# Optimization experiments

Hardware: AMD Instinct MI355X
Metric: run time of the kernel (lower is better)

The kernel has to match this reference:

```python
import jax, jax.numpy as jnp
import numpy as np

# Config (matches init_kwargs)
D_MODEL = 1024
D_MLP = 4096
N_EXPERTS = 8
TOP_K = 2  # experts_per_token
BATCH = 1
POS = 2048


def setup_inputs() -> dict:
    key = jax.random.key(0)
    k0, k1, k2, k3, k4 = jax.random.split(key, 5)
    s = 0.02  # typical init scale
    x = jax.random.normal(k0, (BATCH, POS, D_MODEL), jnp.float32)
    W_gate = jax.random.normal(k1, (D_MODEL, N_EXPERTS), jnp.float32) * s  # router
    We_gate = jax.random.normal(k2, (N_EXPERTS, D_MODEL, D_MLP), jnp.float32) * s
    We_in = jax.random.normal(k3, (N_EXPERTS, D_MODEL, D_MLP), jnp.float32) * s
    We_out = jax.random.normal(k4, (N_EXPERTS, D_MLP, D_MODEL), jnp.float32) * s
    return {"x": x, "W_gate": W_gate, "We_gate": We_gate, "We_in": We_in, "We_out": We_out}


def reference(x, W_gate, We_gate, We_in, We_out):
    B, P, D = x.shape
    T = B * P
    E = W_gate.shape[1]
    h = x.reshape(T, D)  # [T, D]

    # Router: logits -> fp32 softmax -> top-k -> renormalize (as in torch code)
    logits = h @ W_gate  # [T, E]
    probs = jax.nn.softmax(logits.astype(jnp.float32), axis=-1)
    topw, topi = jax.lax.top_k(probs, TOP_K)  # [T, K]
    topw = topw / jnp.sum(topw, axis=-1, keepdims=True)
    topw = topw.astype(x.dtype)

    # Per-token combine weight for each expert (0 if not routed). [T, E]
    w_full = jnp.zeros((T, E), x.dtype).at[jnp.arange(T)[:, None], topi].add(topw)

    # Gated-MLP per expert; scan over the small fixed expert axis to avoid
    # materializing [E, T, D_MLP] hidden states at once.
    def per_expert(acc, params):
        Wg, Wi, Wo, we = params  # Wg/Wi: [D, D_MLP], Wo: [D_MLP, D], we: [T]
        hid = jax.nn.silu(h @ Wg) * (h @ Wi)  # [T, D_MLP]
        return acc + (hid @ Wo) * we[:, None], None

    res, _ = jax.lax.scan(
        per_expert,
        jnp.zeros((T, D), x.dtype),
        (We_gate, We_in, We_out, w_full.T),
    )
    return res.reshape(B, P, D)
```

## Files before the change

kernel.cpp:

```cpp
#include <hip/hip_runtime.h>
#include <hip/hip_bf16.h>

#define T_TOK 2048
#define DMODEL 1024
#define DMLP 4096
#define NEXP 8
#define YB 4

typedef __bf16 bf16x8 __attribute__((ext_vector_type(8)));
typedef float f32x4 __attribute__((ext_vector_type(4)));
typedef unsigned short u16x8 __attribute__((ext_vector_type(8)));

__device__ __forceinline__ unsigned short f2bf(float f) {
  return __builtin_bit_cast(unsigned short, (__bf16)f);
}

__global__ __launch_bounds__(64) void router_k(
    const float* __restrict__ x, const float* __restrict__ wg,
    int* __restrict__ topi, float* __restrict__ topw) {
  int t = blockIdx.x;
  int lane = threadIdx.x;
  const float* hx = x + (size_t)t * DMODEL;
  float acc[NEXP];
#pragma unroll
  for (int e = 0; e < NEXP; ++e) acc[e] = 0.f;
  for (int i = lane; i < DMODEL; i += 64) {
    float xi = hx[i];
    const float* w = wg + (size_t)i * NEXP;
#pragma unroll
    for (int e = 0; e < NEXP; ++e) acc[e] += xi * w[e];
  }
#pragma unroll
  for (int off = 32; off > 0; off >>= 1) {
#pragma unroll
    for (int e = 0; e < NEXP; ++e) acc[e] += __shfl_down(acc[e], off);
  }
  if (lane == 0) {
    float m = acc[0];
#pragma unroll
    for (int e = 1; e < NEXP; ++e) m = fmaxf(m, acc[e]);
    float p[NEXP], s = 0.f;
#pragma unroll
    for (int e = 0; e < NEXP; ++e) { p[e] = expf(acc[e] - m); s += p[e]; }
    float inv = 1.f / s;
#pragma unroll
    for (int e = 0; e < NEXP; ++e) p[e] *= inv;
    int i1 = 0;
#pragma unroll
    for (int e = 1; e < NEXP; ++e) if (p[e] > p[i1]) i1 = e;
    int i2 = (i1 == 0) ? 1 : 0;
#pragma unroll
    for (int e = 0; e < NEXP; ++e) if (e != i1 && p[e] > p[i2]) i2 = e;
    float w1 = p[i1], w2 = p[i2];
    float rs = 1.f / (w1 + w2);
    topi[2 * t] = i1;
    topi[2 * t + 1] = i2;
    topw[2 * t] = w1 * rs;
    topw[2 * t + 1] = w2 * rs;
  }
}

__global__ __launch_bounds__(512) void compact_k(
    const int* __restrict__ topi, const float* __restrict__ topw,
    int* __restrict__ offsets, int* __restrict__ perm,
    float* __restrict__ wrow) {
  int tid = threadIdx.x;
  int w = tid >> 6, lane = tid & 63;
  __shared__ int hist[NEXP][NEXP];
  __shared__ int base_s[NEXP][NEXP];
  unsigned long long ltmask = (lane == 63) ? ~0ULL >> 1 : ((1ULL << lane) - 1ULL);

  int c[NEXP];
#pragma unroll
  for (int ex = 0; ex < NEXP; ++ex) c[ex] = 0;
  for (int it = 0; it < 8; ++it) {
    int j = w * 512 + it * 64 + lane;
    int e = topi[j];
#pragma unroll
    for (int ex = 0; ex < NEXP; ++ex) {
      unsigned long long m = __ballot(e == ex);
      c[ex] += __popcll(m);
    }
  }
  if (lane == 0) {
#pragma unroll
    for (int ex = 0; ex < NEXP; ++ex) hist[w][ex] = c[ex];
  }
  __syncthreads();
  if (tid == 0) {
    int s = 0;
    for (int ex = 0; ex < NEXP; ++ex) {
      offsets[ex] = s;
      int t = s;
      for (int w2 = 0; w2 < NEXP; ++w2) { base_s[w2][ex] = t; t += hist[w2][ex]; }
      s = t;
    }
    offsets[NEXP] = s;
  }
  __syncthreads();
  int rb[NEXP];
#pragma unroll
  for (int ex = 0; ex < NEXP; ++ex) rb[ex] = base_s[w][ex];
  for (int it = 0; it < 8; ++it) {
    int j = w * 512 + it * 64 + lane;
    int e = topi[j];
    float pw = topw[j];
#pragma unroll
    for (int ex = 0; ex < NEXP; ++ex) {
      unsigned long long m = __ballot(e == ex);
      if (e == ex) {
        int p = rb[ex] + __popcll(m & ltmask);
        perm[p] = j >> 1;
        wrow[p] = pw;
      }
      rb[ex] += __popcll(m);
    }
  }
}

#define BPITCH 40

__global__ __launch_bounds__(256) void hid_k(
    const float* __restrict__ x, const float* __restrict__ weg,
    const float* __restrict__ wei, const int* __restrict__ offsets,
    const int* __restrict__ perm, const float* __restrict__ wrow,
    unsigned short* __restrict__ hid) {
  int e = blockIdx.z;
  int off = offsets[e], cnt = offsets[e + 1] - off;
  int nb = blockIdx.x * 64;
  const float* wg = weg + (size_t)e * DMODEL * DMLP;
  const float* wi = wei + (size_t)e * DMODEL * DMLP;

  __shared__ unsigned short As[128 * BPITCH];
  __shared__ unsigned short Bg[64 * BPITCH];
  __shared__ unsigned short Bi[64 * BPITCH];

  int tid = threadIdx.x;
  int lane = tid & 63, wid = tid >> 6;
  int wm = (wid & 1) * 64, wn = (wid >> 1) * 32;
  int lr = lane & 15, q = lane >> 4;

  int bn = tid & 63, kq = tid >> 6;
  const float* gsrc = wg + (size_t)(kq * 8) * DMLP + nb + bn;
  const float* isrc = wi + (size_t)(kq * 8) * DMLP + nb + bn;
  int bdst = bn * BPITCH + kq * 8;

  for (int m0 = blockIdx.y * 128; m0 < cnt; m0 += YB * 128) {
    const float* aptr[4];
    int adst[4];
#pragma unroll
    for (int it = 0; it < 4; ++it) {
      int task = tid + it * 256;
      int r = task >> 3, kc = (task & 7) * 4;
      int pl = m0 + r;
      int src = perm[off + ((pl < cnt) ? pl : 0)];
      aptr[it] = x + (size_t)src * DMODEL + kc;
      adst[it] = r * BPITCH + kc;
    }

    f32x4 accg[4][2], acci[4][2];
    f32x4 z = {0.f, 0.f, 0.f, 0.f};
#pragma unroll
    for (int i = 0; i < 4; ++i)
#pragma unroll
      for (int j = 0; j < 2; ++j) { accg[i][j] = z; acci[i][j] = z; }

    for (int k0 = 0; k0 < DMODEL; k0 += 32) {
#pragma unroll
      for (int it = 0; it < 4; ++it) {
        float4 v = *(const float4*)(aptr[it] + k0);
        ushort4 u;
        u.x = f2bf(v.x); u.y = f2bf(v.y); u.z = f2bf(v.z); u.w = f2bf(v.w);
        *(ushort4*)(&As[adst[it]]) = u;
      }
      {
        const float* pg = gsrc + (size_t)k0 * DMLP;
        const float* pi = isrc + (size_t)k0 * DMLP;
        float gv[8], iv[8];
#pragma unroll
        for (int kr = 0; kr < 8; ++kr) {
          gv[kr] = pg[(size_t)kr * DMLP];
          iv[kr] = pi[(size_t)kr * DMLP];
        }
        u16x8 ug, ui;
#pragma unroll
        for (int kr = 0; kr < 8; ++kr) {
          ug[kr] = f2bf(gv[kr]);
          ui[kr] = f2bf(iv[kr]);
        }
        *(u16x8*)(&Bg[bdst]) = ug;
        *(u16x8*)(&Bi[bdst]) = ui;
      }
      __syncthreads();
      bf16x8 af[4], bgf[2], bif[2];
#pragma unroll
      for (int i = 0; i < 4; ++i)
        af[i] = *(const bf16x8*)(&As[(wm + i * 16 + lr) * BPITCH + q * 8]);
#pragma unroll
      for (int j = 0; j < 2; ++j) {
        bgf[j] = *(const bf16x8*)(&Bg[(wn + j * 16 + lr) * BPITCH + q * 8]);
        bif[j] = *(const bf16x8*)(&Bi[(wn + j * 16 + lr) * BPITCH + q * 8]);
      }
#pragma unroll
      for (int i = 0; i < 4; ++i)
#pragma unroll
        for (int j = 0; j < 2; ++j) {
          accg[i][j] = __builtin_amdgcn_mfma_f32_16x16x32_bf16(af[i], bgf[j], accg[i][j], 0, 0, 0);
          acci[i][j] = __builtin_amdgcn_mfma_f32_16x16x32_bf16(af[i], bif[j], acci[i][j], 0, 0, 0);
        }
      __syncthreads();
    }
#pragma unroll
    for (int i = 0; i < 4; ++i)
#pragma unroll
      for (int j = 0; j < 2; ++j)
#pragma unroll
        for (int r = 0; r < 4; ++r) {
          int row = wm + i * 16 + q * 4 + r;
          int pl = m0 + row;
          if (pl < cnt) {
            int pos = off + pl;
            float g = accg[i][j][r], vv = acci[i][j][r];
            float hv = (g / (1.f + expf(-g))) * vv * wrow[pos];
            hid[(size_t)pos * DMLP + nb + wn + j * 16 + lr] = f2bf(hv);
          }
        }
  }
}

__global__ __launch_bounds__(256) void out_k(
    const unsigned short* __restrict__ hid, const float* __restrict__ weo,
    const int* __restrict__ offsets, const int* __restrict__ perm,
    float* __restrict__ out) {
  int e = blockIdx.z;
  int off = offsets[e], cnt = offsets[e + 1] - off;
  int kh = blockIdx.y & 1;
  int yb = blockIdx.y >> 1;
  int nb = blockIdx.x * 64;
  const float* wo = weo + (size_t)e * DMLP * DMODEL;

  __shared__ unsigned short As[128 * BPITCH];
  __shared__ unsigned short Bs[64 * BPITCH];

  int tid = threadIdx.x;
  int lane = tid & 63, wid = tid >> 6;
  int wm = (wid & 1) * 64, wn = (wid >> 1) * 32;
  int lr = lane & 15, q = lane >> 4;

  int bn = tid & 63, kq = tid >> 6;
  const float* bsrc = wo + (size_t)(kh * 2048 + kq * 8) * DMODEL + nb + bn;
  int bdst = bn * BPITCH + kq * 8;

  for (int m0 = yb * 128; m0 < cnt; m0 += YB * 128) {
    const unsigned short* aptr[2];
    int adst[2];
#pragma unroll
    for (int it = 0; it < 2; ++it) {
      int task = tid + it * 256;
      int r = task >> 2, kg = (task & 3) * 8;
      int pl = m0 + r;
      int src = off + ((pl < cnt) ? pl : 0);
      aptr[it] = hid + (size_t)src * DMLP + kh * 2048 + kg;
      adst[it] = r * BPITCH + kg;
    }

    f32x4 acc[4][2];
    f32x4 z = {0.f, 0.f, 0.f, 0.f};
#pragma unroll
    for (int i = 0; i < 4; ++i)
#pragma unroll
      for (int j = 0; j < 2; ++j) acc[i][j] = z;

    for (int kk = 0; kk < 2048; kk += 32) {
#pragma unroll
      for (int it = 0; it < 2; ++it) {
        uint4 v = *(const uint4*)(aptr[it] + kk);
        *(uint4*)(&As[adst[it]]) = v;
      }
      {
        const float* pb = bsrc + (size_t)kk * DMODEL;
        float bv[8];
#pragma unroll
        for (int kr = 0; kr < 8; ++kr) bv[kr] = pb[(size_t)kr * DMODEL];
        u16x8 ub;
#pragma unroll
        for (int kr = 0; kr < 8; ++kr) ub[kr] = f2bf(bv[kr]);
        *(u16x8*)(&Bs[bdst]) = ub;
      }
      __syncthreads();
      bf16x8 af[4], bfr[2];
#pragma unroll
      for (int i = 0; i < 4; ++i)
        af[i] = *(const bf16x8*)(&As[(wm + i * 16 + lr) * BPITCH + q * 8]);
#pragma unroll
      for (int j = 0; j < 2; ++j)
        bfr[j] = *(const bf16x8*)(&Bs[(wn + j * 16 + lr) * BPITCH + q * 8]);
#pragma unroll
      for (int i = 0; i < 4; ++i)
#pragma unroll
        for (int j = 0; j < 2; ++j)
          acc[i][j] = __builtin_amdgcn_mfma_f32_16x16x32_bf16(af[i], bfr[j], acc[i][j], 0, 0, 0);
      __syncthreads();
    }
#pragma unroll
    for (int i = 0; i < 4; ++i)
#pragma unroll
      for (int j = 0; j < 2; ++j)
#pragma unroll
        for (int r = 0; r < 4; ++r) {
          int row = wm + i * 16 + q * 4 + r;
          int pl = m0 + row;
          if (pl < cnt) {
            int tok = perm[off + pl];
            atomicAdd(&out[(size_t)tok * DMODEL + nb + wn + j * 16 + lr],
                      acc[i][j][r]);
          }
        }
  }
}

extern "C" void kernel_launch(void* const* d_in, const int* in_sizes, int n_in,
                              void* d_out, int out_size, void* d_ws,
                              size_t ws_size, hipStream_t stream) {
  const float* x = (const float*)d_in[0];
  const float* wgate = (const float*)d_in[1];
  const float* weg = (const float*)d_in[2];
  const float* wei = (const float*)d_in[3];
  const float* weo = (const float*)d_in[4];
  float* out = (float*)d_out;

  char* ws = (char*)d_ws;
  int* topi = (int*)(ws + 0);
  float* topw = (float*)(ws + (16 << 10));
  int* offsets = (int*)(ws + (32 << 10));
  int* perm = (int*)(ws + (33 << 10));
  float* wrow = (float*)(ws + (49 << 10));
  unsigned short* hid = (unsigned short*)(ws + (65 << 10));

  hipMemsetAsync(d_out, 0, (size_t)out_size * sizeof(float), stream);
  router_k<<<dim3(T_TOK), dim3(64), 0, stream>>>(x, wgate, topi, topw);
  compact_k<<<dim3(1), dim3(512), 0, stream>>>(topi, topw, offsets, perm, wrow);
  hid_k<<<dim3(DMLP / 64, YB, NEXP), dim3(256), 0, stream>>>(
      x, weg, wei, offsets, perm, wrow, hid);
  out_k<<<dim3(DMODEL / 64, 2 * YB, NEXP), dim3(256), 0, stream>>>(
      hid, weo, offsets, perm, out);
}
```

Baseline: 720.8 us.

## Pre-convert weights and gathered activations to bf16 and load via global_load_lds

Adds prepass kernels that gather the routed token rows of x into a contiguous bf16 buffer and transpose the expert weights into bf16 K-major layout in workspace. The GEMM kernels then fill shared memory with 16-byte direct global-to-LDS loads instead of strided fp32 loads plus in-loop conversion, and out_k drops its split-K. This trades extra full-weight transpose passes and workspace traffic on every call for simpler, coalesced GEMM inner loops. A fallback path with improved fp32 B loads runs when the workspace is too small.

```diff
diff --git a/kernel.cpp b/kernel.cpp
--- a/kernel.cpp
+++ b/kernel.cpp
@@ -5,14 +5,21 @@
 #define DMODEL 1024
 #define DMLP 4096
 #define NEXP 8
+#define TOTROW (2 * T_TOK)
 #define YB 4
 
 typedef __bf16 bf16x8 __attribute__((ext_vector_type(8)));
 typedef float f32x4 __attribute__((ext_vector_type(4)));
-typedef unsigned short u16x8 __attribute__((ext_vector_type(8)));
 
 __device__ __forceinline__ unsigned short f2bf(float f) {
   return __builtin_bit_cast(unsigned short, (__bf16)f);
+}
+
+__device__ __forceinline__ void gl2lds16(const unsigned short* g,
+                                         unsigned short* l) {
+  __builtin_amdgcn_global_load_lds(
+      (const __attribute__((address_space(1))) unsigned int*)(const void*)g,
+      (__attribute__((address_space(3))) unsigned int*)(void*)l, 16, 0, 0);
 }
 
 __global__ __launch_bounds__(64) void router_k(
@@ -68,7 +75,7 @@
   int w = tid >> 6, lane = tid & 63;
   __shared__ int hist[NEXP][NEXP];
   __shared__ int base_s[NEXP][NEXP];
-  unsigned long long ltmask = (lane == 63) ? ~0ULL >> 1 : ((1ULL << lane) - 1ULL);
+  unsigned long long ltmask = (1ULL << lane) - 1ULL;
 
   int c[NEXP];
 #pragma unroll
@@ -118,45 +125,88 @@
   }
 }
 
-#define BPITCH 40
+__global__ __launch_bounds__(256) void gather_x_k(
+    const float* __restrict__ x, const int* __restrict__ perm,
+    unsigned short* __restrict__ abf) {
+  int p = blockIdx.x;
+  int src = perm[p];
+  int c = threadIdx.x * 4;
+  float4 v = *(const float4*)(x + (size_t)src * DMODEL + c);
+  ushort4 u;
+  u.x = f2bf(v.x); u.y = f2bf(v.y); u.z = f2bf(v.z); u.w = f2bf(v.w);
+  *(ushort4*)(&abf[(size_t)p * DMODEL + c]) = u;
+}
+
+#define TP 68
+__global__ __launch_bounds__(256) void transw_k(
+    const float* __restrict__ src, unsigned short* __restrict__ dst,
+    int K, int N) {
+  __shared__ __align__(16) unsigned short sm[64 * TP];
+  int e = blockIdx.z;
+  int kt = blockIdx.y * 64, nt = blockIdx.x * 64;
+  const float* s = src + (size_t)e * K * N;
+  unsigned short* d = dst + (size_t)e * N * K;
+  int tid = threadIdx.x;
+  int r0 = tid >> 4, c0 = (tid & 15) * 4;
+#pragma unroll
+  for (int rr = 0; rr < 4; ++rr) {
+    int k = r0 + rr * 16;
+    float4 v = *(const float4*)(s + (size_t)(kt + k) * N + nt + c0);
+    ushort4 u;
+    u.x = f2bf(v.x); u.y = f2bf(v.y); u.z = f2bf(v.z); u.w = f2bf(v.w);
+    *(ushort4*)(&sm[k * TP + c0]) = u;
+  }
+  __syncthreads();
+#pragma unroll
+  for (int rr = 0; rr < 4; ++rr) {
+    int n = r0 + rr * 16;
+    ushort4 u;
+    u.x = sm[(c0 + 0) * TP + n];
+    u.y = sm[(c0 + 1) * TP + n];
+    u.z = sm[(c0 + 2) * TP + n];
+    u.w = sm[(c0 + 3) * TP + n];
+    *(ushort4*)(&d[(size_t)(nt + n) * K + kt + c0]) = u;
+  }
+}
 
 __global__ __launch_bounds__(256) void hid_k(
-    const float* __restrict__ x, const float* __restrict__ weg,
-    const float* __restrict__ wei, const int* __restrict__ offsets,
-    const int* __restrict__ perm, const float* __restrict__ wrow,
+    const unsigned short* __restrict__ abf,
+    const unsigned short* __restrict__ wgt,
+    const unsigned short* __restrict__ wit,
+    const int* __restrict__ offsets, const float* __restrict__ wrow,
     unsigned short* __restrict__ hid) {
   int e = blockIdx.z;
   int off = offsets[e], cnt = offsets[e + 1] - off;
   int nb = blockIdx.x * 64;
-  const float* wg = weg + (size_t)e * DMODEL * DMLP;
-  const float* wi = wei + (size_t)e * DMODEL * DMLP;
-
-  __shared__ unsigned short As[128 * BPITCH];
-  __shared__ unsigned short Bg[64 * BPITCH];
-  __shared__ unsigned short Bi[64 * BPITCH];
+  const unsigned short* wge = wgt + (size_t)e * DMLP * DMODEL;
+  const unsigned short* wie = wit + (size_t)e * DMLP * DMODEL;
+
+  __shared__ __align__(16) unsigned short As[128 * 32];
+  __shared__ __align__(16) unsigned short Bg[64 * 32];
+  __shared__ __align__(16) unsigned short Bi[64 * 32];
 
   int tid = threadIdx.x;
   int lane = tid & 63, wid = tid >> 6;
   int wm = (wid & 1) * 64, wn = (wid >> 1) * 32;
   int lr = lane & 15, q = lane >> 4;
-
-  int bn = tid & 63, kq = tid >> 6;
-  const float* gsrc = wg + (size_t)(kq * 8) * DMLP + nb + bn;
-  const float* isrc = wi + (size_t)(kq * 8) * DMLP + nb + bn;
-  int bdst = bn * BPITCH + kq * 8;
+  int sr = lane >> 2, ko = lane & 3;
+
+  const unsigned short* gSrc =
+      wge + (size_t)(nb + wid * 16 + sr) * DMODEL + ko * 8;
+  const unsigned short* iSrc =
+      wie + (size_t)(nb + wid * 16 + sr) * DMODEL + ko * 8;
+  unsigned short* ldsA0 = As + wid * 1024;
+  unsigned short* ldsA1 = As + wid * 1024 + 512;
+  unsigned short* ldsBg = Bg + wid * 512;
+  unsigned short* ldsBi = Bi + wid * 512;
 
   for (int m0 = blockIdx.y * 128; m0 < cnt; m0 += YB * 128) {
-    const float* aptr[4];
-    int adst[4];
-#pragma unroll
-    for (int it = 0; it < 4; ++it) {
-      int task = tid + it * 256;
-      int r = task >> 3, kc = (task & 7) * 4;
-      int pl = m0 + r;
-      int src = perm[off + ((pl < cnt) ? pl : 0)];
-      aptr[it] = x + (size_t)src * DMODEL + kc;
-      adst[it] = r * BPITCH + kc;
-    }
+    int ra = off + m0 + wid * 32 + sr;
+    int rb = ra + 16;
+    ra = ra < (TOTROW - 1) ? ra : (TOTROW - 1);
+    rb = rb < (TOTROW - 1) ? rb : (TOTROW - 1);
+    const unsigned short* aSrc0 = abf + (size_t)ra * DMODEL + ko * 8;
+    const unsigned short* aSrc1 = abf + (size_t)rb * DMODEL + ko * 8;
 
     f32x4 accg[4][2], acci[4][2];
     f32x4 z = {0.f, 0.f, 0.f, 0.f};
@@ -166,47 +216,28 @@
       for (int j = 0; j < 2; ++j) { accg[i][j] = z; acci[i][j] = z; }
 
     for (int k0 = 0; k0 < DMODEL; k0 += 32) {
-#pragma unroll
-      for (int it = 0; it < 4; ++it) {
-        float4 v = *(const float4*)(aptr[it] + k0);
-        ushort4 u;
-        u.x = f2bf(v.x); u.y = f2bf(v.y); u.z = f2bf(v.z); u.w = f2bf(v.w);
-        *(ushort4*)(&As[adst[it]]) = u;
-      }
-      {
-        const float* pg = gsrc + (size_t)k0 * DMLP;
-        const float* pi = isrc + (size_t)k0 * DMLP;
-        float gv[8], iv[8];
-#pragma unroll
-        for (int kr = 0; kr < 8; ++kr) {
-          gv[kr] = pg[(size_t)kr * DMLP];
-          iv[kr] = pi[(size_t)kr * DMLP];
-        }
-        u16x8 ug, ui;
-#pragma unroll
-        for (int kr = 0; kr < 8; ++kr) {
-          ug[kr] = f2bf(gv[kr]);
-          ui[kr] = f2bf(iv[kr]);
-        }
-        *(u16x8*)(&Bg[bdst]) = ug;
-        *(u16x8*)(&Bi[bdst]) = ui;
-      }
+      gl2lds16(aSrc0 + k0, ldsA0);
+      gl2lds16(aSrc1 + k0, ldsA1);
+      gl2lds16(gSrc + k0, ldsBg);
+      gl2lds16(iSrc + k0, ldsBi);
       __syncthreads();
       bf16x8 af[4], bgf[2], bif[2];
 #pragma unroll
       for (int i = 0; i < 4; ++i)
-        af[i] = *(const bf16x8*)(&As[(wm + i * 16 + lr) * BPITCH + q * 8]);
+        af[i] = *(const bf16x8*)(&As[(wm + i * 16 + lr) * 32 + q * 8]);
 #pragma unroll
       for (int j = 0; j < 2; ++j) {
-        bgf[j] = *(const bf16x8*)(&Bg[(wn + j * 16 + lr) * BPITCH + q * 8]);
-        bif[j] = *(const bf16x8*)(&Bi[(wn + j * 16 + lr) * BPITCH + q * 8]);
+        bgf[j] = *(const bf16x8*)(&Bg[(wn + j * 16 + lr) * 32 + q * 8]);
+        bif[j] = *(const bf16x8*)(&Bi[(wn + j * 16 + lr) * 32 + q * 8]);
       }
 #pragma unroll
       for (int i = 0; i < 4; ++i)
 #pragma unroll
         for (int j = 0; j < 2; ++j) {
-          accg[i][j] = __builtin_amdgcn_mfma_f32_16x16x32_bf16(af[i], bgf[j], accg[i][j], 0, 0, 0);
-          acci[i][j] = __builtin_amdgcn_mfma_f32_16x16x32_bf16(af[i], bif[j], acci[i][j], 0, 0, 0);
+          accg[i][j] = __builtin_amdgcn_mfma_f32_16x16x32_bf16(
+              af[i], bgf[j], accg[i][j], 0, 0, 0);
+          acci[i][j] = __builtin_amdgcn_mfma_f32_16x16x32_bf16(
+              af[i], bif[j], acci[i][j], 0, 0, 0);
         }
       __syncthreads();
     }
@@ -229,40 +260,37 @@
 }
 
 __global__ __launch_bounds__(256) void out_k(
-    const unsigned short* __restrict__ hid, const float* __restrict__ weo,
+    const unsigned short* __restrict__ hid,
+    const unsigned short* __restrict__ wot,
     const int* __restrict__ offsets, const int* __restrict__ perm,
     float* __restrict__ out) {
   int e = blockIdx.z;
   int off = offsets[e], cnt = offsets[e + 1] - off;
-  int kh = blockIdx.y & 1;
-  int yb = blockIdx.y >> 1;
   int nb = blockIdx.x * 64;
-  const float* wo = weo + (size_t)e * DMLP * DMODEL;
-
-  __shared__ unsigned short As[128 * BPITCH];
-  __shared__ unsigned short Bs[64 * BPITCH];
+  const unsigned short* woe = wot + (size_t)e * DMLP * DMODEL;
+
+  __shared__ __align__(16) unsigned short As[128 * 32];
+  __shared__ __align__(16) unsigned short Bs[64 * 32];
 
   int tid = threadIdx.x;
   int lane = tid & 63, wid = tid >> 6;
   int wm = (wid & 1) * 64, wn = (wid >> 1) * 32;
   int lr = lane & 15, q = lane >> 4;
-
-  int bn = tid & 63, kq = tid >> 6;
-  const float* bsrc = wo + (size_t)(kh * 2048 + kq * 8) * DMODEL + nb + bn;
-  int bdst = bn * BPITCH + kq * 8;
-
-  for (int m0 = yb * 128; m0 < cnt; m0 += YB * 128) {
-    const unsigned short* aptr[2];
-    int adst[2];
-#pragma unroll
-    for (int it = 0; it < 2; ++it) {
-      int task = tid + it * 256;
-      int r = task >> 2, kg = (task & 3) * 8;
-      int pl = m0 + r;
-      int src = off + ((pl < cnt) ? pl : 0);
-      aptr[it] = hid + (size_t)src * DMLP + kh * 2048 + kg;
-      adst[it] = r * BPITCH + kg;
-    }
+  int sr = lane >> 2, ko = lane & 3;
+
+  const unsigned short* bSrc =
+      woe + (size_t)(nb + wid * 16 + sr) * DMLP + ko * 8;
+  unsigned short* ldsA0 = As + wid * 1024;
+  unsigned short* ldsA1 = As + wid * 1024 + 512;
+  unsigned short* ldsB = Bs + wid * 512;
+
+  for (int m0 = blockIdx.y * 128; m0 < cnt; m0 += YB * 128) {
+    int ra = off + m0 + wid * 32 + sr;
+    int rb = ra + 16;
+    ra = ra < (TOTROW - 1) ? ra : (TOTROW - 1);
+    rb = rb < (TOTROW - 1) ? rb : (TOTROW - 1);
+    const unsigned short* aSrc0 = hid + (size_t)ra * DMLP + ko * 8;
+    const unsigned short* aSrc1 = hid + (size_t)rb * DMLP + ko * 8;
 
     f32x4 acc[4][2];
     f32x4 z = {0.f, 0.f, 0.f, 0.f};
@@ -271,35 +299,24 @@
 #pragma unroll
       for (int j = 0; j < 2; ++j) acc[i][j] = z;
 
-    for (int kk = 0; kk < 2048; kk += 32) {
-#pragma unroll
-      for (int it = 0; it < 2; ++it) {
-        uint4 v = *(const uint4*)(aptr[it] + kk);
-        *(uint4*)(&As[adst[it]]) = v;
-      }
-      {
-        const float* pb = bsrc + (size_t)kk * DMODEL;
-        float bv[8];
-#pragma unroll
-        for (int kr = 0; kr < 8; ++kr) bv[kr] = pb[(size_t)kr * DMODEL];
-        u16x8 ub;
-#pragma unroll
-        for (int kr = 0; kr < 8; ++kr) ub[kr] = f2bf(bv[kr]);
-        *(u16x8*)(&Bs[bdst]) = ub;
-      }
+    for (int kk = 0; kk < DMLP; kk += 32) {
+      gl2lds16(aSrc0 + kk, ldsA0);
+      gl2lds16(aSrc1 + kk, ldsA1);
+      gl2lds16(bSrc + kk, ldsB);
       __syncthreads();
       bf16x8 af[4], bfr[2];
 #pragma unroll
       for (int i = 0; i < 4; ++i)
-        af[i] = *(const bf16x8*)(&As[(wm + i * 16 + lr) * BPITCH + q * 8]);
+        af[i] = *(const bf16x8*)(&As[(wm + i * 16 + lr) * 32 + q * 8]);
 #pragma unroll
       for (int j = 0; j < 2; ++j)
-        bfr[j] = *(const bf16x8*)(&Bs[(wn + j * 16 + lr) * BPITCH + q * 8]);
+        bfr[j] = *(const bf16x8*)(&Bs[(wn + j * 16 + lr) * 32 + q * 8]);
 #pragma unroll
       for (int i = 0; i < 4; ++i)
 #pragma unroll
         for (int j = 0; j < 2; ++j)
-          acc[i][j] = __builtin_amdgcn_mfma_f32_16x16x32_bf16(af[i], bfr[j], acc[i][j], 0, 0, 0);
+          acc[i][j] = __builtin_amdgcn_mfma_f32_16x16x32_bf16(
+              af[i], bfr[j], acc[i][j], 0, 0, 0);
       __syncthreads();
     }
 #pragma unroll
@@ -319,6 +336,192 @@
   }
 }
 
+#define BPITCH 40
+__global__ __launch_bounds__(256) void hid_fb(
+    const float* __restrict__ x, const float* __restrict__ weg,
+    const float* __restrict__ wei, const int* __restrict__ offsets,
+    const int* __restrict__ perm, const float* __restrict__ wrow,
+    unsigned short* __restrict__ hid) {
+  int e = blockIdx.z;
+  int off = offsets[e], end = offsets[e + 1];
+  int cnt = end - off;
+  int m0 = blockIdx.y * 128;
+  if (m0 >= cnt) return;
+  int nb = blockIdx.x * 64;
+  const float* wg = weg + (size_t)e * DMODEL * DMLP;
+  const float* wi = wei + (size_t)e * DMODEL * DMLP;
+  __shared__ unsigned short As[128 * BPITCH];
+  __shared__ unsigned short Bg[64 * BPITCH];
+  __shared__ unsigned short Bi[64 * BPITCH];
+  int tid = threadIdx.x;
+  int lane = tid & 63, wid = tid >> 6;
+  int wm = (wid & 1) * 64, wn = (wid >> 1) * 32;
+  int lr = lane & 15, q = lane >> 4;
+  f32x4 accg[4][2], acci[4][2];
+  f32x4 z = {0.f, 0.f, 0.f, 0.f};
+#pragma unroll
+  for (int i = 0; i < 4; ++i)
+#pragma unroll
+    for (int j = 0; j < 2; ++j) { accg[i][j] = z; acci[i][j] = z; }
+  const float* aptr[4];
+  int adst[4];
+#pragma unroll
+  for (int it = 0; it < 4; ++it) {
+    int task = tid + it * 256;
+    int r = task >> 3, kc = (task & 7) * 4;
+    int pl = m0 + r;
+    int src = perm[off + ((pl < cnt) ? pl : 0)];
+    aptr[it] = x + (size_t)src * DMODEL + kc;
+    adst[it] = r * BPITCH + kc;
+  }
+  int tn = (tid & 15) * 4, tk = (tid >> 4) * 2;
+  for (int k0 = 0; k0 < DMODEL; k0 += 32) {
+#pragma unroll
+    for (int it = 0; it < 4; ++it) {
+      float4 v = *(const float4*)(aptr[it] + k0);
+      ushort4 u;
+      u.x = f2bf(v.x); u.y = f2bf(v.y); u.z = f2bf(v.z); u.w = f2bf(v.w);
+      *(ushort4*)(&As[adst[it]]) = u;
+    }
+    {
+      const float* pg = wg + (size_t)(k0 + tk) * DMLP + nb + tn;
+      float4 g0 = *(const float4*)(pg);
+      float4 g1 = *(const float4*)(pg + DMLP);
+      const float* pi = wi + (size_t)(k0 + tk) * DMLP + nb + tn;
+      float4 i0 = *(const float4*)(pi);
+      float4 i1 = *(const float4*)(pi + DMLP);
+      const float* c0 = (const float*)&g0;
+      const float* c1 = (const float*)&g1;
+      const float* d0 = (const float*)&i0;
+      const float* d1 = (const float*)&i1;
+#pragma unroll
+      for (int cix = 0; cix < 4; ++cix) {
+        ushort2 vg; vg.x = f2bf(c0[cix]); vg.y = f2bf(c1[cix]);
+        *(ushort2*)(&Bg[(tn + cix) * BPITCH + tk]) = vg;
+        ushort2 vi; vi.x = f2bf(d0[cix]); vi.y = f2bf(d1[cix]);
+        *(ushort2*)(&Bi[(tn + cix) * BPITCH + tk]) = vi;
+      }
+    }
+    __syncthreads();
+    bf16x8 af[4], bgf[2], bif[2];
+#pragma unroll
+    for (int i = 0; i < 4; ++i)
+      af[i] = *(const bf16x8*)(&As[(wm + i * 16 + lr) * BPITCH + q * 8]);
+#pragma unroll
+    for (int j = 0; j < 2; ++j) {
+      bgf[j] = *(const bf16x8*)(&Bg[(wn + j * 16 + lr) * BPITCH + q * 8]);
+      bif[j] = *(const bf16x8*)(&Bi[(wn + j * 16 + lr) * BPITCH + q * 8]);
+    }
+#pragma unroll
+    for (int i = 0; i < 4; ++i)
+#pragma unroll
+      for (int j = 0; j < 2; ++j) {
+        accg[i][j] = __builtin_amdgcn_mfma_f32_16x16x32_bf16(af[i], bgf[j], accg[i][j], 0, 0, 0);
+        acci[i][j] = __builtin_amdgcn_mfma_f32_16x16x32_bf16(af[i], bif[j], acci[i][j], 0, 0, 0);
+      }
+    __syncthreads();
+  }
+#pragma unroll
+  for (int i = 0; i < 4; ++i)
+#pragma unroll
+    for (int j = 0; j < 2; ++j)
+#pragma unroll
+      for (int r = 0; r < 4; ++r) {
+        int row = wm + i * 16 + q * 4 + r;
+        int pl = m0 + row;
+        if (pl < cnt) {
+          int pos = off + pl;
+          float g = accg[i][j][r], vv = acci[i][j][r];
+          float hv = (g / (1.f + expf(-g))) * vv * wrow[pos];
+          hid[(size_t)pos * DMLP + nb + wn + j * 16 + lr] = f2bf(hv);
+        }
+      }
+}
+
+__global__ __launch_bounds__(256) void out_fb(
+    const unsigned short* __restrict__ hid, const float* __restrict__ weo,
+    const int* __restrict__ offsets, const int* __restrict__ perm,
+    float* __restrict__ out) {
+  int e = blockIdx.z;
+  int off = offsets[e], end = offsets[e + 1];
+  int cnt = end - off;
+  int m0 = blockIdx.y * 128;
+  if (m0 >= cnt) return;
+  int nb = blockIdx.x * 64;
+  const float* wo = weo + (size_t)e * DMLP * DMODEL;
+  __shared__ unsigned short As[128 * BPITCH];
+  __shared__ unsigned short Bs[64 * BPITCH];
+  int tid = threadIdx.x;
+  int lane = tid & 63, wid = tid >> 6;
+  int wm = (wid & 1) * 64, wn = (wid >> 1) * 32;
+  int lr = lane & 15, q = lane >> 4;
+  f32x4 acc[4][2];
+  f32x4 z = {0.f, 0.f, 0.f, 0.f};
+#pragma unroll
+  for (int i = 0; i < 4; ++i)
+#pragma unroll
+    for (int j = 0; j < 2; ++j) acc[i][j] = z;
+  const unsigned short* aptr[2];
+  int adst[2];
+#pragma unroll
+  for (int it = 0; it < 2; ++it) {
+    int task = tid + it * 256;
+    int r = task >> 2, kg = (task & 3) * 8;
+    int pl = m0 + r;
+    int src = off + ((pl < cnt) ? pl : 0);
+    aptr[it] = hid + (size_t)src * DMLP + kg;
+    adst[it] = r * BPITCH + kg;
+  }
+  int tn = (tid & 15) * 4, tk = (tid >> 4) * 2;
+  for (int k0 = 0; k0 < DMLP; k0 += 32) {
+#pragma unroll
+    for (int it = 0; it < 2; ++it) {
+      uint4 v = *(const uint4*)(aptr[it] + k0);
+      *(uint4*)(&As[adst[it]]) = v;
+    }
+    {
+      const float* pb = wo + (size_t)(k0 + tk) * DMODEL + nb + tn;
+      float4 b0 = *(const float4*)(pb);
+      float4 b1 = *(const float4*)(pb + DMODEL);
+      const float* c0 = (const float*)&b0;
+      const float* c1 = (const float*)&b1;
+#pragma unroll
+      for (int cix = 0; cix < 4; ++cix) {
+        ushort2 vb; vb.x = f2bf(c0[cix]); vb.y = f2bf(c1[cix]);
+        *(ushort2*)(&Bs[(tn + cix) * BPITCH + tk]) = vb;
+      }
+    }
+    __syncthreads();
+    bf16x8 af[4], bfr[2];
+#pragma unroll
+    for (int i = 0; i < 4; ++i)
+      af[i] = *(const bf16x8*)(&As[(wm + i * 16 + lr) * BPITCH + q * 8]);
+#pragma unroll
+    for (int j = 0; j < 2; ++j)
+      bfr[j] = *(const bf16x8*)(&Bs[(wn + j * 16 + lr) * BPITCH + q * 8]);
+#pragma unroll
+    for (int i = 0; i < 4; ++i)
+#pragma unroll
+      for (int j = 0; j < 2; ++j)
+        acc[i][j] = __builtin_amdgcn_mfma_f32_16x16x32_bf16(af[i], bfr[j], acc[i][j], 0, 0, 0);
+    __syncthreads();
+  }
+#pragma unroll
+  for (int i = 0; i < 4; ++i)
+#pragma unroll
+    for (int j = 0; j < 2; ++j)
+#pragma unroll
+      for (int r = 0; r < 4; ++r) {
+        int row = wm + i * 16 + q * 4 + r;
+        int pl = m0 + row;
+        if (pl < cnt) {
+          int tok = perm[off + pl];
+          atomicAdd(&out[(size_t)tok * DMODEL + nb + wn + j * 16 + lr],
+                    acc[i][j][r]);
+        }
+      }
+}
+
 extern "C" void kernel_launch(void* const* d_in, const int* in_sizes, int n_in,
                               void* d_out, int out_size, void* d_ws,
                               size_t ws_size, hipStream_t stream) {
@@ -335,13 +538,35 @@
   int* offsets = (int*)(ws + (32 << 10));
   int* perm = (int*)(ws + (33 << 10));
   float* wrow = (float*)(ws + (49 << 10));
-  unsigned short* hid = (unsigned short*)(ws + (65 << 10));
+  const size_t MB = 1ull << 20;
+  unsigned short* abf = (unsigned short*)(ws + 128 * 1024);
+  unsigned short* hid = (unsigned short*)(ws + 8 * MB + 128 * 1024);
+  unsigned short* wgt = (unsigned short*)(ws + 40 * MB + 128 * 1024);
+  unsigned short* wit = (unsigned short*)(ws + 104 * MB + 128 * 1024);
+  unsigned short* wot = wgt;
+  const size_t need = 168 * MB + 128 * 1024;
 
   hipMemsetAsync(d_out, 0, (size_t)out_size * sizeof(float), stream);
   router_k<<<dim3(T_TOK), dim3(64), 0, stream>>>(x, wgate, topi, topw);
   compact_k<<<dim3(1), dim3(512), 0, stream>>>(topi, topw, offsets, perm, wrow);
-  hid_k<<<dim3(DMLP / 64, YB, NEXP), dim3(256), 0, stream>>>(
-      x, weg, wei, offsets, perm, wrow, hid);
-  out_k<<<dim3(DMODEL / 64, 2 * YB, NEXP), dim3(256), 0, stream>>>(
-      hid, weo, offsets, perm, out);
-}
+
+  if (ws_size >= need) {
+    gather_x_k<<<dim3(TOTROW), dim3(256), 0, stream>>>(x, perm, abf);
+    transw_k<<<dim3(DMLP / 64, DMODEL / 64, NEXP), dim3(256), 0, stream>>>(
+        weg, wgt, DMODEL, DMLP);
+    transw_k<<<dim3(DMLP / 64, DMODEL / 64, NEXP), dim3(256), 0, stream>>>(
+        wei, wit, DMODEL, DMLP);
+    hid_k<<<dim3(DMLP / 64, YB, NEXP), dim3(256), 0, stream>>>(
+        abf, wgt, wit, offsets, wrow, hid);
+    transw_k<<<dim3(DMODEL / 64, DMLP / 64, NEXP), dim3(256), 0, stream>>>(
+        weo, wot, DMLP, DMODEL);
+    out_k<<<dim3(DMODEL / 64, YB, NEXP), dim3(256), 0, stream>>>(
+        hid, wot, offsets, perm, out);
+  } else {
+    unsigned short* hid_s = (unsigned short*)(ws + (65 << 10));
+    hid_fb<<<dim3(DMLP / 64, T_TOK / 128, NEXP), dim3(256), 0, stream>>>(
+        x, weg, wei, offsets, perm, wrow, hid_s);
+    out_fb<<<dim3(DMODEL / 64, T_TOK / 128, NEXP), dim3(256), 0, stream>>>(
+        hid_s, weo, offsets, perm, out);
+  }
+}
```

Result: slower. 748.3 us (+3.8%).
